# Kernel optimization log

Measured on AMD Instinct MI355X. Metric: run time of the kernel, lower is better.

The kernel has to match this reference:

```python
import jax, jax.numpy as jnp
import numpy as np

N, E, F_IN, F_EDGE, HID, OUT = 100000, 1600000, 128, 8, 128, 2
BN_EPS = 1e-5


def setup_inputs() -> dict:
    key = jax.random.key(0)
    ks = jax.random.split(key, 16)
    rn = lambda k, shape, s=0.05: jax.random.normal(k, shape, jnp.float32) * s
    return {
        "x": jax.random.normal(ks[0], (N, F_IN), jnp.float32),
        "edge_attr": jax.random.uniform(ks[1], (E, F_EDGE), dtype=jnp.float32),
        "edge_index": jax.random.randint(ks[2], (2, E), 0, N, jnp.int32),
        # edge MLP: Linear(F_EDGE, HID) -> ReLU -> Linear(HID, 1) -> Sigmoid
        "ew1_w": rn(ks[3], (F_EDGE, HID)), "ew1_b": jnp.zeros((HID,), jnp.float32),
        "ew2_w": rn(ks[4], (HID, 1)), "ew2_b": jnp.zeros((1,), jnp.float32),
        # SAGEConv layers: lin_l (on aggregated neighbors, with bias) + lin_r (root)
        "w1_l": rn(ks[5], (F_IN, HID)), "b1_l": jnp.zeros((HID,), jnp.float32), "w1_r": rn(ks[6], (F_IN, HID)),
        "w2_l": rn(ks[7], (HID, HID)), "b2_l": jnp.zeros((HID,), jnp.float32), "w2_r": rn(ks[8], (HID, HID)),
        "w3_l": rn(ks[9], (HID, OUT)), "b3_l": jnp.zeros((OUT,), jnp.float32), "w3_r": rn(ks[10], (HID, OUT)),
        # BatchNorm1d (eval mode: running stats)
        "bn1_g": jnp.ones((HID,), jnp.float32), "bn1_b": jnp.zeros((HID,), jnp.float32),
        "bn1_m": rn(ks[11], (HID,), 0.01), "bn1_v": jnp.ones((HID,), jnp.float32),
        "bn2_g": jnp.ones((HID,), jnp.float32), "bn2_b": jnp.zeros((HID,), jnp.float32),
        "bn2_m": rn(ks[12], (HID,), 0.01), "bn2_v": jnp.ones((HID,), jnp.float32),
    }


def _sage(x, src, dst, ew, w_l, b_l, w_r):
    # PyG SAGEConv(aggr='mean'): msg = x[src] * edge_weight, mean over incoming edges at dst
    msg = x[src] * ew[:, None]                                  # [E, F]
    s = jax.ops.segment_sum(msg, dst, num_segments=N)           # [N, F]
    deg = jax.ops.segment_sum(jnp.ones((src.shape[0],), x.dtype), dst, num_segments=N)
    agg = s / jnp.maximum(deg, 1.0)[:, None]
    return agg @ w_l + b_l + x @ w_r


def _bn_eval(h, g, b, m, v):
    return (h - m) * jax.lax.rsqrt(v + BN_EPS) * g + b


def reference(x, edge_attr, edge_index,
              ew1_w, ew1_b, ew2_w, ew2_b,
              w1_l, b1_l, w1_r, w2_l, b2_l, w2_r, w3_l, b3_l, w3_r,
              bn1_g, bn1_b, bn1_m, bn1_v, bn2_g, bn2_b, bn2_m, bn2_v):
    src, dst = edge_index[0], edge_index[1]
    # per-edge scalar weight from small MLP
    ew = jax.nn.sigmoid(jax.nn.relu(edge_attr @ ew1_w + ew1_b) @ ew2_w + ew2_b).reshape(-1)
    h = _sage(x, src, dst, ew, w1_l, b1_l, w1_r)
    h = jax.nn.relu(_bn_eval(h, bn1_g, bn1_b, bn1_m, bn1_v))    # dropout no-op in eval
    h = _sage(h, src, dst, ew, w2_l, b2_l, w2_r)
    h = jax.nn.relu(_bn_eval(h, bn2_g, bn2_b, bn2_m, bn2_v))
    return _sage(h, src, dst, ew, w3_l, b3_l, w3_r)
```

## Files before the change

### kernel.cpp

```cpp
#include <hip/hip_runtime.h>
#include <math.h>

#define N_NODES 100000
#define N_EDGES 1600000
#define F_INF   128
#define HIDF    128

typedef __attribute__((ext_vector_type(8)))  short short8;
typedef __attribute__((ext_vector_type(16))) float floatx16;

__device__ __forceinline__ unsigned short f2bf(float f) {
    unsigned u = __float_as_uint(f);
    return (unsigned short)((u + 0x7FFFu + ((u >> 16) & 1u)) >> 16);
}

__global__ __launch_bounds__(256) void k_edge_mlp(
        const float* __restrict__ ea,
        const float* __restrict__ w1, const float* __restrict__ b1,
        const float* __restrict__ w2, const float* __restrict__ b2,
        float* __restrict__ ew) {
    const int lane = threadIdx.x & 63;
    const int cl   = lane & 31;
    const int half = lane >> 5;
    const int wid  = blockIdx.x * (blockDim.x >> 6) + (threadIdx.x >> 6);
    const int nw   = gridDim.x * (blockDim.x >> 6);

    short8 bw[4];
    float  w2c[4];
#pragma unroll
    for (int cb = 0; cb < 4; ++cb) {
        const int n = cb * 32 + cl;
        short8 b;
        if (half == 0) {
#pragma unroll
            for (int j = 0; j < 8; ++j) b[j] = (short)f2bf(w1[j * 128 + n]);
        } else {
            b[0] = (short)f2bf(b1[n]);
#pragma unroll
            for (int j = 1; j < 8; ++j) b[j] = 0;
        }
        bw[cb] = b;
        w2c[cb] = w2[n];
    }
    short8 Abias;
    Abias[0] = (short)0x3F80;
#pragma unroll
    for (int j = 1; j < 8; ++j) Abias[j] = 0;

    floatx16 czero;
#pragma unroll
    for (int r = 0; r < 16; ++r) czero[r] = 0.f;

    const float bias2 = b2[0];

    for (int e0 = wid * 32; e0 < N_EDGES; e0 += nw * 32) {
        short8 Ah;
        if (half == 0) {
            const float4 a0 = *(const float4*)(ea + (size_t)(e0 + cl) * 8);
            const float4 a1 = *(const float4*)(ea + (size_t)(e0 + cl) * 8 + 4);
            Ah[0] = (short)f2bf(a0.x); Ah[1] = (short)f2bf(a0.y);
            Ah[2] = (short)f2bf(a0.z); Ah[3] = (short)f2bf(a0.w);
            Ah[4] = (short)f2bf(a1.x); Ah[5] = (short)f2bf(a1.y);
            Ah[6] = (short)f2bf(a1.z); Ah[7] = (short)f2bf(a1.w);
        } else {
            Ah = Abias;
        }

        float z[16];
#pragma unroll
        for (int r = 0; r < 16; ++r) z[r] = 0.f;

#pragma unroll
        for (int cb = 0; cb < 4; ++cb) {
            floatx16 acc = __builtin_amdgcn_mfma_f32_32x32x16_bf16(Ah, bw[cb], czero, 0, 0, 0);
#pragma unroll
            for (int r = 0; r < 16; ++r)
                z[r] = fmaf(fmaxf(acc[r], 0.f), w2c[cb], z[r]);
        }

#pragma unroll
        for (int m = 1; m <= 16; m <<= 1) {
#pragma unroll
            for (int r = 0; r < 16; ++r) z[r] += __shfl_xor(z[r], m, 64);
        }

        float zz = z[0];
#pragma unroll
        for (int r = 1; r < 16; ++r) zz = (cl == r) ? z[r] : zz;
        if (cl < 16) {
            const int row = (cl & 3) + 8 * (cl >> 2) + 4 * half;
            ew[e0 + row] = 1.f / (1.f + __expf(-(zz + bias2)));
        }
    }
}

__global__ void k_deg(const int* __restrict__ dst, int* __restrict__ deg,
                      unsigned char* __restrict__ rank) {
    int e = blockIdx.x * 256 + threadIdx.x;
    if (e < N_EDGES) rank[e] = (unsigned char)atomicAdd(&deg[dst[e]], 1);
}

__global__ void k_scan1(const int* __restrict__ deg, int* __restrict__ incl,
                        int* __restrict__ bsum) {
    __shared__ int sm[1024];
    const int tid = threadIdx.x;
    const int gi  = blockIdx.x * 1024 + tid;
    int v = (gi < N_NODES) ? deg[gi] : 0;
    sm[tid] = v;
    __syncthreads();
    for (int off = 1; off < 1024; off <<= 1) {
        int t = (tid >= off) ? sm[tid - off] : 0;
        __syncthreads();
        sm[tid] += t;
        __syncthreads();
    }
    if (gi < N_NODES) incl[gi] = sm[tid];
    if (tid == 1023) bsum[blockIdx.x] = sm[1023];
}

__global__ void k_scan2(const int* __restrict__ bsum, int* __restrict__ boff, int nb) {
    __shared__ int sm[128];
    const int tid = threadIdx.x;
    int v = (tid < nb) ? bsum[tid] : 0;
    sm[tid] = v;
    __syncthreads();
    for (int off = 1; off < 128; off <<= 1) {
        int t = (tid >= off) ? sm[tid - off] : 0;
        __syncthreads();
        sm[tid] += t;
        __syncthreads();
    }
    boff[tid] = sm[tid] - v;
}

__global__ void k_scan3(const int* __restrict__ incl, const int* __restrict__ boff,
                        int* __restrict__ rowptr) {
    int i = blockIdx.x * 256 + threadIdx.x;
    if (i < N_NODES) rowptr[i + 1] = boff[i >> 10] + incl[i];
    if (i == 0) rowptr[0] = 0;
}

__global__ void k_fill(const int* __restrict__ src, const int* __restrict__ dst,
                       const float* __restrict__ ew, const int* __restrict__ rowptr,
                       const unsigned char* __restrict__ rank,
                       unsigned* __restrict__ cw) {
    int e = blockIdx.x * 256 + threadIdx.x;
    if (e < N_EDGES) {
        int d   = dst[e];
        int pos = rowptr[d] + (int)rank[e];
        unsigned wb = (unsigned)f2bf(ew[e]) & 0x7FFFu;
        cw[pos] = ((unsigned)src[e] << 15) | wb;
    }
}

__global__ void k_cast(const float* __restrict__ x, unsigned short* __restrict__ xb) {
    const int i = (blockIdx.x * 256 + threadIdx.x) * 4;
    const float4 v = *(const float4*)(x + i);
    ushort4 o;
    o.x = f2bf(v.x); o.y = f2bf(v.y); o.z = f2bf(v.z); o.w = f2bf(v.w);
    *(ushort4*)(xb + i) = o;
}

__global__ __launch_bounds__(256) void k_agg16(
        const unsigned short* __restrict__ xb, const int* __restrict__ rowptr,
        const unsigned* __restrict__ cw, float* __restrict__ aggout) {
    const int lane = threadIdx.x & 63;
    const int half = lane >> 5;
    const int cl   = lane & 31;
    const int node = blockIdx.x * (blockDim.x >> 6) + (threadIdx.x >> 6);
    if (node >= N_NODES) return;
    const int s = rowptr[node], e = rowptr[node + 1];
    float a0 = 0.f, a1 = 0.f, a2 = 0.f, a3 = 0.f;

    for (int j0 = s; j0 < e; j0 += 8) {
        int ss[4]; float ww[4];
#pragma unroll
        for (int u = 0; u < 4; ++u) {
            const int j  = j0 + 2 * u + half;
            const int jc = min(j, e - 1);
            const unsigned p = cw[jc];
            ss[u] = (int)(p >> 15);
            ww[u] = (j < e) ? __uint_as_float((p & 0x7FFFu) << 16) : 0.f;
        }
        uint2 g[4];
#pragma unroll
        for (int u = 0; u < 4; ++u)
            g[u] = *(const uint2*)(xb + (size_t)ss[u] * 128 + cl * 4);
#pragma unroll
        for (int u = 0; u < 4; ++u) {
            const float f0 = __uint_as_float(g[u].x << 16);
            const float f1 = __uint_as_float(g[u].x & 0xFFFF0000u);
            const float f2 = __uint_as_float(g[u].y << 16);
            const float f3 = __uint_as_float(g[u].y & 0xFFFF0000u);
            a0 = fmaf(ww[u], f0, a0);
            a1 = fmaf(ww[u], f1, a1);
            a2 = fmaf(ww[u], f2, a2);
            a3 = fmaf(ww[u], f3, a3);
        }
    }
    a0 += __shfl_xor(a0, 32, 64);
    a1 += __shfl_xor(a1, 32, 64);
    a2 += __shfl_xor(a2, 32, 64);
    a3 += __shfl_xor(a3, 32, 64);
    if (half == 0) {
        const float inv = 1.f / fmaxf((float)(e - s), 1.f);
        float4 r;
        r.x = a0 * inv; r.y = a1 * inv; r.z = a2 * inv; r.w = a3 * inv;
        *(float4*)(aggout + (size_t)node * 128 + cl * 4) = r;
    }
}

__global__ void k_wpack(const float* __restrict__ Wl, const float* __restrict__ Wr,
                        short* __restrict__ Whi, short* __restrict__ Wlo) {
    int idx = blockIdx.x * 256 + threadIdx.x;
    int j  = idx & 7;
    int L  = (idx >> 3) & 63;
    int cb = (idx >> 9) & 3;
    int kb = (idx >> 11);
    int k  = kb * 16 + (L >> 5) * 8 + j;
    int n  = cb * 32 + (L & 31);
    float a = (k < 128) ? Wl[k * 128 + n] : Wr[(k - 128) * 128 + n];
    unsigned short hb = f2bf(a);
    float hf = __uint_as_float((unsigned)hb << 16);
    Whi[idx] = (short)hb;
    Wlo[idx] = (short)f2bf(a - hf);
}

__global__ __launch_bounds__(256) void k_gemm_mfma(
    const float* __restrict__ Aagg, const float* __restrict__ Ax,
    const short* __restrict__ Whi, const short* __restrict__ Wlo,
    const float* __restrict__ bl,
    const float* __restrict__ bng, const float* __restrict__ bnb,
    const float* __restrict__ bnm, const float* __restrict__ bnv,
    float* __restrict__ out, unsigned short* __restrict__ out16) {
    const int tid  = threadIdx.x;
    const int lane = tid & 63;
    const int w    = tid >> 6;
    const int row0 = blockIdx.x * 128 + w * 32;
    const int rrow = lane & 31;
    const int kq   = lane >> 5;
    const int arow = min(row0 + rrow, N_NODES - 1);

    floatx16 acc[4];
#pragma unroll
    for (int cb = 0; cb < 4; ++cb)
#pragma unroll
        for (int r = 0; r < 16; ++r) acc[cb][r] = 0.f;

    const float* Abase0 = Aagg + (size_t)arow * 128 + kq * 8;
    const float* Abase1 = Ax   + (size_t)arow * 128 + kq * 8;

#pragma unroll 2
    for (int kb = 0; kb < 16; ++kb) {
        const float* ap = ((kb < 8) ? Abase0 : Abase1) + (kb & 7) * 16;
        const float4 a0 = *(const float4*)(ap);
        const float4 a1 = *(const float4*)(ap + 4);
        const float av[8] = {a0.x, a0.y, a0.z, a0.w, a1.x, a1.y, a1.z, a1.w};
        short8 Ah, Al;
#pragma unroll
        for (int j = 0; j < 8; ++j) {
            unsigned short hb = f2bf(av[j]);
            float hf = __uint_as_float((unsigned)hb << 16);
            Ah[j] = (short)hb;
            Al[j] = (short)f2bf(av[j] - hf);
        }
#pragma unroll
        for (int cb = 0; cb < 4; ++cb) {
            const size_t wo = ((size_t)(kb * 4 + cb) * 64 + lane) * 8;
            const short8 wh = *(const short8*)(Whi + wo);
            const short8 wl = *(const short8*)(Wlo + wo);
            acc[cb] = __builtin_amdgcn_mfma_f32_32x32x16_bf16(Ah, wh, acc[cb], 0, 0, 0);
            acc[cb] = __builtin_amdgcn_mfma_f32_32x32x16_bf16(Al, wh, acc[cb], 0, 0, 0);
            acc[cb] = __builtin_amdgcn_mfma_f32_32x32x16_bf16(Ah, wl, acc[cb], 0, 0, 0);
        }
    }

#pragma unroll
    for (int cb = 0; cb < 4; ++cb) {
        const int c = cb * 32 + (lane & 31);
        const float s = bng[c] * rsqrtf(bnv[c] + 1e-5f);
        const float t = (bl[c] - bnm[c]) * s + bnb[c];
#pragma unroll
        for (int r = 0; r < 16; ++r) {
            const int row = row0 + (r & 3) + 8 * (r >> 2) + 4 * kq;
            if (row < N_NODES) {
                const float v = fmaxf(fmaf(acc[cb][r], s, t), 0.f);
                out[(size_t)row * 128 + c] = v;
                if (out16) out16[(size_t)row * 128 + c] = f2bf(v);
            }
        }
    }
}

__global__ void k_lin3(const float* __restrict__ h, const float* __restrict__ w3l,
                       const float* __restrict__ w3r, float* __restrict__ t4) {
    const int lane = threadIdx.x & 63;
    const int node = blockIdx.x * (blockDim.x >> 6) + (threadIdx.x >> 6);
    if (node >= N_NODES) return;
    float h0 = h[(size_t)node * 128 + lane];
    float h1 = h[(size_t)node * 128 + 64 + lane];
    float2 wl0 = *(const float2*)(w3l + lane * 2);
    float2 wl1 = *(const float2*)(w3l + (64 + lane) * 2);
    float2 wr0 = *(const float2*)(w3r + lane * 2);
    float2 wr1 = *(const float2*)(w3r + (64 + lane) * 2);
    float p0 = h0 * wl0.x + h1 * wl1.x;
    float p1 = h0 * wl0.y + h1 * wl1.y;
    float p2 = h0 * wr0.x + h1 * wr1.x;
    float p3 = h0 * wr0.y + h1 * wr1.y;
#pragma unroll
    for (int m = 1; m < 64; m <<= 1) {
        p0 += __shfl_xor(p0, m, 64);
        p1 += __shfl_xor(p1, m, 64);
        p2 += __shfl_xor(p2, m, 64);
        p3 += __shfl_xor(p3, m, 64);
    }
    if (lane == 0) {
        float4 o; o.x = p0; o.y = p1; o.z = p2; o.w = p3;
        *(float4*)(t4 + (size_t)node * 4) = o;
    }
}

__global__ void k_out(const float* __restrict__ t4, const int* __restrict__ rowptr,
                      const unsigned* __restrict__ cw,
                      const float* __restrict__ b3, float* __restrict__ out) {
    const int lane = threadIdx.x & 63;
    const int node = blockIdx.x * (blockDim.x >> 6) + (threadIdx.x >> 6);
    if (node >= N_NODES) return;
    const int s = rowptr[node], e = rowptr[node + 1];
    float a0 = 0.f, a1 = 0.f;
    for (int j = s + lane; j < e; j += 64) {
        const unsigned p = cw[j];
        const int   sr = (int)(p >> 15);
        const float w  = __uint_as_float((p & 0x7FFFu) << 16);
        float2 t = *(const float2*)(t4 + (size_t)sr * 4);
        a0 += w * t.x; a1 += w * t.y;
    }
#pragma unroll
    for (int m = 1; m < 64; m <<= 1) {
        a0 += __shfl_xor(a0, m, 64);
        a1 += __shfl_xor(a1, m, 64);
    }
    if (lane == 0) {
        float inv = 1.f / fmaxf((float)(e - s), 1.f);
        float2 o;
        o.x = a0 * inv + b3[0] + t4[(size_t)node * 4 + 2];
        o.y = a1 * inv + b3[1] + t4[(size_t)node * 4 + 3];
        *(float2*)(out + (size_t)node * 2) = o;
    }
}

extern "C" void kernel_launch(void* const* d_in, const int* in_sizes, int n_in,
                              void* d_out, int out_size, void* d_ws, size_t ws_size,
                              hipStream_t stream) {
    const float* x    = (const float*)d_in[0];
    const float* ea   = (const float*)d_in[1];
    const int*   ei   = (const int*)d_in[2];
    const float* ew1w = (const float*)d_in[3];
    const float* ew1b = (const float*)d_in[4];
    const float* ew2w = (const float*)d_in[5];
    const float* ew2b = (const float*)d_in[6];
    const float* w1l  = (const float*)d_in[7];
    const float* b1l  = (const float*)d_in[8];
    const float* w1r  = (const float*)d_in[9];
    const float* w2l  = (const float*)d_in[10];
    const float* b2l  = (const float*)d_in[11];
    const float* w2r  = (const float*)d_in[12];
    const float* w3l  = (const float*)d_in[13];
    const float* b3l  = (const float*)d_in[14];
    const float* w3r  = (const float*)d_in[15];
    const float* bn1g = (const float*)d_in[16];
    const float* bn1b = (const float*)d_in[17];
    const float* bn1m = (const float*)d_in[18];
    const float* bn1v = (const float*)d_in[19];
    const float* bn2g = (const float*)d_in[20];
    const float* bn2b = (const float*)d_in[21];
    const float* bn2m = (const float*)d_in[22];
    const float* bn2v = (const float*)d_in[23];

    const int* src = ei;
    const int* dst = ei + N_EDGES;
    float* out = (float*)d_out;

    size_t off = 0;
    auto carve = [&](size_t bytes) -> void* {
        void* p = (char*)d_ws + off;
        off += (bytes + 255) & ~(size_t)255;
        return p;
    };
    float* ew     = (float*)carve((size_t)N_EDGES * 4);
    unsigned* cw  = (unsigned*)carve((size_t)N_EDGES * 4);
    unsigned char* rank = (unsigned char*)carve((size_t)N_EDGES);
    int*   rowptr = (int*)carve((size_t)(N_NODES + 1) * 4);
    int*   deg    = (int*)carve((size_t)N_NODES * 4);
    int*   bsum   = (int*)carve(128 * 4);
    int*   boff   = (int*)carve(128 * 4);
    int*   incl   = (int*)carve((size_t)N_NODES * 4);
    float* agg    = (float*)carve((size_t)N_NODES * 128 * 4);
    float* hA     = (float*)carve((size_t)N_NODES * 128 * 4);
    float* hB     = (float*)carve((size_t)N_NODES * 128 * 4);
    float* t4     = (float*)carve((size_t)N_NODES * 4 * 4);
    short* W1hi   = (short*)carve(32768 * 2);
    short* W1lo   = (short*)carve(32768 * 2);
    short* W2hi   = (short*)carve(32768 * 2);
    short* W2lo   = (short*)carve(32768 * 2);
    unsigned short* xb   = (unsigned short*)carve((size_t)N_NODES * 128 * 2);
    unsigned short* hA16 = (unsigned short*)carve((size_t)N_NODES * 128 * 2);
    (void)ws_size; (void)n_in; (void)in_sizes; (void)out_size;

    hipMemsetAsync(deg, 0, (size_t)N_NODES * 4, stream);

    const int EB = (N_EDGES + 255) / 256;
    const int NB_SCAN = (N_NODES + 1023) / 1024;
    const int NWB = (N_NODES + 3) / 4;
    const int GB = (N_NODES + 127) / 128;
    const int CB = (N_NODES * 128 / 4 + 255) / 256;

    k_deg<<<EB, 256, 0, stream>>>(dst, deg, rank);
    k_cast<<<CB, 256, 0, stream>>>(x, xb);
    k_edge_mlp<<<2048, 256, 0, stream>>>(ea, ew1w, ew1b, ew2w, ew2b, ew);
    k_wpack<<<128, 256, 0, stream>>>(w1l, w1r, W1hi, W1lo);
    k_wpack<<<128, 256, 0, stream>>>(w2l, w2r, W2hi, W2lo);
    k_scan1<<<NB_SCAN, 1024, 0, stream>>>(deg, incl, bsum);
    k_scan2<<<1, 128, 0, stream>>>(bsum, boff, NB_SCAN);
    k_scan3<<<(N_NODES + 255) / 256, 256, 0, stream>>>(incl, boff, rowptr);
    k_fill<<<EB, 256, 0, stream>>>(src, dst, ew, rowptr, rank, cw);

    k_agg16<<<NWB, 256, 0, stream>>>(xb, rowptr, cw, agg);
    k_gemm_mfma<<<GB, 256, 0, stream>>>(agg, x, W1hi, W1lo, b1l,
                                        bn1g, bn1b, bn1m, bn1v, hA, hA16);
    k_agg16<<<NWB, 256, 0, stream>>>(hA16, rowptr, cw, agg);
    k_gemm_mfma<<<GB, 256, 0, stream>>>(agg, hA, W2hi, W2lo, b2l,
                                        bn2g, bn2b, bn2m, bn2v, hB, nullptr);
    k_lin3<<<NWB, 256, 0, stream>>>(hB, w3l, w3r, t4);
    k_out<<<NWB, 256, 0, stream>>>(t4, rowptr, cw, b3l, out);
}
```

Before: 591.5 us.

## Fuse front-end kernels and store activations as split bf16 hi/lo pairs

Merges the degree count, x cast, edge MLP and both weight packs into one heterogeneous kernel that dispatches on block index. Scan2 and scan3 are merged into one kernel. All intermediate activations (agg, hA, hB) are now stored as bf16 hi/lo pairs instead of fp32, so the GEMM loads ready-made MFMA operands and no longer converts them. The goals are fewer launches and less conversion work inside the GEMM. Total bytes are roughly unchanged, and the fused kernel mixes workloads that may balance unevenly.

New measurement: 562.6 us. 4.9% less time.

```diff
diff --git a/kernel.cpp b/kernel.cpp
--- a/kernel.cpp
+++ b/kernel.cpp
@@ -6,6 +6,11 @@
 #define F_INF   128
 #define HIDF    128
 
+#define MLP_BLOCKS  2048
+#define CAST_BLOCKS 12500
+#define WP_BASE     (CAST_BLOCKS + MLP_BLOCKS)
+#define FRONT_GRID  (WP_BASE + 256)
+
 typedef __attribute__((ext_vector_type(8)))  short short8;
 typedef __attribute__((ext_vector_type(16))) float floatx16;
 
@@ -13,17 +18,70 @@
     unsigned u = __float_as_uint(f);
     return (unsigned short)((u + 0x7FFFu + ((u >> 16) & 1u)) >> 16);
 }
-
-__global__ __launch_bounds__(256) void k_edge_mlp(
+__device__ __forceinline__ float bf2f(unsigned short h) {
+    return __uint_as_float((unsigned)h << 16);
+}
+
+__global__ __launch_bounds__(256) void k_front(
+        const float* __restrict__ x,
+        unsigned short* __restrict__ xbHi, unsigned short* __restrict__ xbLo,
+        const int* __restrict__ dst, int* __restrict__ deg,
+        unsigned char* __restrict__ rank,
         const float* __restrict__ ea,
-        const float* __restrict__ w1, const float* __restrict__ b1,
-        const float* __restrict__ w2, const float* __restrict__ b2,
-        float* __restrict__ ew) {
+        const float* __restrict__ mw1, const float* __restrict__ mb1,
+        const float* __restrict__ mw2, const float* __restrict__ mb2,
+        float* __restrict__ ew,
+        const float* __restrict__ w1l, const float* __restrict__ w1r,
+        short* __restrict__ W1hi, short* __restrict__ W1lo,
+        const float* __restrict__ w2l, const float* __restrict__ w2r,
+        short* __restrict__ W2hi, short* __restrict__ W2lo) {
+    const int bid = blockIdx.x;
+
+    if (bid >= WP_BASE) {
+        const int wb  = bid - WP_BASE;
+        const int idx = (wb & 127) * 256 + threadIdx.x;
+        const float* Wl = (wb < 128) ? w1l : w2l;
+        const float* Wr = (wb < 128) ? w1r : w2r;
+        short* Whi = (wb < 128) ? W1hi : W2hi;
+        short* Wlo = (wb < 128) ? W1lo : W2lo;
+        const int j  = idx & 7;
+        const int L  = (idx >> 3) & 63;
+        const int cb = (idx >> 9) & 3;
+        const int kb = (idx >> 11);
+        const int k  = kb * 16 + (L >> 5) * 8 + j;
+        const int n  = cb * 32 + (L & 31);
+        const float a = (k < 128) ? Wl[k * 128 + n] : Wr[(k - 128) * 128 + n];
+        const unsigned short hb = f2bf(a);
+        Whi[idx] = (short)hb;
+        Wlo[idx] = (short)f2bf(a - bf2f(hb));
+        return;
+    }
+
+    const bool is_mlp = ((bid % 7) == 3) && (bid < 7 * MLP_BLOCKS);
+    if (!is_mlp) {
+        const int c   = (bid < 4) ? 0 : min(MLP_BLOCKS, (bid - 4) / 7 + 1);
+        const int gid = (bid - c) * 256 + (int)threadIdx.x;
+        const int i   = gid * 4;
+        const float4 v = *(const float4*)(x + i);
+        ushort4 h, l;
+        h.x = f2bf(v.x); l.x = f2bf(v.x - bf2f(h.x));
+        h.y = f2bf(v.y); l.y = f2bf(v.y - bf2f(h.y));
+        h.z = f2bf(v.z); l.z = f2bf(v.z - bf2f(h.z));
+        h.w = f2bf(v.w); l.w = f2bf(v.w - bf2f(h.w));
+        *(ushort4*)(xbHi + i) = h;
+        *(ushort4*)(xbLo + i) = l;
+        if ((gid & 1) == 0) {
+            const int e = gid >> 1;
+            rank[e] = (unsigned char)atomicAdd(&deg[dst[e]], 1);
+        }
+        return;
+    }
+
     const int lane = threadIdx.x & 63;
     const int cl   = lane & 31;
     const int half = lane >> 5;
-    const int wid  = blockIdx.x * (blockDim.x >> 6) + (threadIdx.x >> 6);
-    const int nw   = gridDim.x * (blockDim.x >> 6);
+    const int wid  = (bid / 7) * 4 + ((int)threadIdx.x >> 6);
+    const int nw   = MLP_BLOCKS * 4;
 
     short8 bw[4];
     float  w2c[4];
@@ -33,14 +91,14 @@
         short8 b;
         if (half == 0) {
 #pragma unroll
-            for (int j = 0; j < 8; ++j) b[j] = (short)f2bf(w1[j * 128 + n]);
+            for (int j = 0; j < 8; ++j) b[j] = (short)f2bf(mw1[j * 128 + n]);
         } else {
-            b[0] = (short)f2bf(b1[n]);
+            b[0] = (short)f2bf(mb1[n]);
 #pragma unroll
             for (int j = 1; j < 8; ++j) b[j] = 0;
         }
         bw[cb] = b;
-        w2c[cb] = w2[n];
+        w2c[cb] = mw2[n];
     }
     short8 Abias;
     Abias[0] = (short)0x3F80;
@@ -51,7 +109,7 @@
 #pragma unroll
     for (int r = 0; r < 16; ++r) czero[r] = 0.f;
 
-    const float bias2 = b2[0];
+    const float bias2 = mb2[0];
 
     for (int e0 = wid * 32; e0 < N_EDGES; e0 += nw * 32) {
         short8 Ah;
@@ -92,12 +150,6 @@
             ew[e0 + row] = 1.f / (1.f + __expf(-(zz + bias2)));
         }
     }
-}
-
-__global__ void k_deg(const int* __restrict__ dst, int* __restrict__ deg,
-                      unsigned char* __restrict__ rank) {
-    int e = blockIdx.x * 256 + threadIdx.x;
-    if (e < N_EDGES) rank[e] = (unsigned char)atomicAdd(&deg[dst[e]], 1);
 }
 
 __global__ void k_scan1(const int* __restrict__ deg, int* __restrict__ incl,
@@ -118,25 +170,27 @@
     if (tid == 1023) bsum[blockIdx.x] = sm[1023];
 }
 
-__global__ void k_scan2(const int* __restrict__ bsum, int* __restrict__ boff, int nb) {
+__global__ void k_scan23(const int* __restrict__ incl, const int* __restrict__ bsum,
+                         int* __restrict__ rowptr, int nb) {
     __shared__ int sm[128];
     const int tid = threadIdx.x;
-    int v = (tid < nb) ? bsum[tid] : 0;
-    sm[tid] = v;
+    int v = 0;
+    if (tid < 128) {
+        v = (tid < nb) ? bsum[tid] : 0;
+        sm[tid] = v;
+    }
     __syncthreads();
     for (int off = 1; off < 128; off <<= 1) {
-        int t = (tid >= off) ? sm[tid - off] : 0;
+        int t = 0;
+        if (tid < 128 && tid >= off) t = sm[tid - off];
         __syncthreads();
-        sm[tid] += t;
+        if (tid < 128) sm[tid] += t;
         __syncthreads();
     }
-    boff[tid] = sm[tid] - v;
-}
-
-__global__ void k_scan3(const int* __restrict__ incl, const int* __restrict__ boff,
-                        int* __restrict__ rowptr) {
-    int i = blockIdx.x * 256 + threadIdx.x;
-    if (i < N_NODES) rowptr[i + 1] = boff[i >> 10] + incl[i];
+    if (tid < 128) sm[tid] -= v;
+    __syncthreads();
+    const int i = blockIdx.x * 256 + tid;
+    if (i < N_NODES) rowptr[i + 1] = sm[i >> 10] + incl[i];
     if (i == 0) rowptr[0] = 0;
 }
 
@@ -153,17 +207,10 @@
     }
 }
 
-__global__ void k_cast(const float* __restrict__ x, unsigned short* __restrict__ xb) {
-    const int i = (blockIdx.x * 256 + threadIdx.x) * 4;
-    const float4 v = *(const float4*)(x + i);
-    ushort4 o;
-    o.x = f2bf(v.x); o.y = f2bf(v.y); o.z = f2bf(v.z); o.w = f2bf(v.w);
-    *(ushort4*)(xb + i) = o;
-}
-
 __global__ __launch_bounds__(256) void k_agg16(
         const unsigned short* __restrict__ xb, const int* __restrict__ rowptr,
-        const unsigned* __restrict__ cw, float* __restrict__ aggout) {
+        const unsigned* __restrict__ cw,
+        unsigned short* __restrict__ aggHi, unsigned short* __restrict__ aggLo) {
     const int lane = threadIdx.x & 63;
     const int half = lane >> 5;
     const int cl   = lane & 31;
@@ -204,35 +251,25 @@
     a3 += __shfl_xor(a3, 32, 64);
     if (half == 0) {
         const float inv = 1.f / fmaxf((float)(e - s), 1.f);
-        float4 r;
-        r.x = a0 * inv; r.y = a1 * inv; r.z = a2 * inv; r.w = a3 * inv;
-        *(float4*)(aggout + (size_t)node * 128 + cl * 4) = r;
-    }
-}
-
-__global__ void k_wpack(const float* __restrict__ Wl, const float* __restrict__ Wr,
-                        short* __restrict__ Whi, short* __restrict__ Wlo) {
-    int idx = blockIdx.x * 256 + threadIdx.x;
-    int j  = idx & 7;
-    int L  = (idx >> 3) & 63;
-    int cb = (idx >> 9) & 3;
-    int kb = (idx >> 11);
-    int k  = kb * 16 + (L >> 5) * 8 + j;
-    int n  = cb * 32 + (L & 31);
-    float a = (k < 128) ? Wl[k * 128 + n] : Wr[(k - 128) * 128 + n];
-    unsigned short hb = f2bf(a);
-    float hf = __uint_as_float((unsigned)hb << 16);
-    Whi[idx] = (short)hb;
-    Wlo[idx] = (short)f2bf(a - hf);
-}
-
-__global__ __launch_bounds__(256) void k_gemm_mfma(
-    const float* __restrict__ Aagg, const float* __restrict__ Ax,
+        a0 *= inv; a1 *= inv; a2 *= inv; a3 *= inv;
+        ushort4 h, l;
+        h.x = f2bf(a0); l.x = f2bf(a0 - bf2f(h.x));
+        h.y = f2bf(a1); l.y = f2bf(a1 - bf2f(h.y));
+        h.z = f2bf(a2); l.z = f2bf(a2 - bf2f(h.z));
+        h.w = f2bf(a3); l.w = f2bf(a3 - bf2f(h.w));
+        *(ushort4*)(aggHi + (size_t)node * 128 + cl * 4) = h;
+        *(ushort4*)(aggLo + (size_t)node * 128 + cl * 4) = l;
+    }
+}
+
+__global__ __launch_bounds__(256) void k_gemm(
+    const unsigned short* __restrict__ AaggHi, const unsigned short* __restrict__ AaggLo,
+    const unsigned short* __restrict__ AxHi, const unsigned short* __restrict__ AxLo,
     const short* __restrict__ Whi, const short* __restrict__ Wlo,
     const float* __restrict__ bl,
     const float* __restrict__ bng, const float* __restrict__ bnb,
     const float* __restrict__ bnm, const float* __restrict__ bnv,
-    float* __restrict__ out, unsigned short* __restrict__ out16) {
+    unsigned short* __restrict__ outHi, unsigned short* __restrict__ outLo) {
     const int tid  = threadIdx.x;
     const int lane = tid & 63;
     const int w    = tid >> 6;
@@ -247,23 +284,13 @@
 #pragma unroll
         for (int r = 0; r < 16; ++r) acc[cb][r] = 0.f;
 
-    const float* Abase0 = Aagg + (size_t)arow * 128 + kq * 8;
-    const float* Abase1 = Ax   + (size_t)arow * 128 + kq * 8;
+    const size_t abase = (size_t)arow * 128 + kq * 8;
 
 #pragma unroll 2
     for (int kb = 0; kb < 16; ++kb) {
-        const float* ap = ((kb < 8) ? Abase0 : Abase1) + (kb & 7) * 16;
-        const float4 a0 = *(const float4*)(ap);
-        const float4 a1 = *(const float4*)(ap + 4);
-        const float av[8] = {a0.x, a0.y, a0.z, a0.w, a1.x, a1.y, a1.z, a1.w};
-        short8 Ah, Al;
-#pragma unroll
-        for (int j = 0; j < 8; ++j) {
-            unsigned short hb = f2bf(av[j]);
-            float hf = __uint_as_float((unsigned)hb << 16);
-            Ah[j] = (short)hb;
-            Al[j] = (short)f2bf(av[j] - hf);
-        }
+        const size_t ao = abase + (kb & 7) * 16;
+        const short8 Ah = *(const short8*)(((kb < 8) ? AaggHi : AxHi) + ao);
+        const short8 Al = *(const short8*)(((kb < 8) ? AaggLo : AxLo) + ao);
 #pragma unroll
         for (int cb = 0; cb < 4; ++cb) {
             const size_t wo = ((size_t)(kb * 4 + cb) * 64 + lane) * 8;
@@ -285,24 +312,28 @@
             const int row = row0 + (r & 3) + 8 * (r >> 2) + 4 * kq;
             if (row < N_NODES) {
                 const float v = fmaxf(fmaf(acc[cb][r], s, t), 0.f);
-                out[(size_t)row * 128 + c] = v;
-                if (out16) out16[(size_t)row * 128 + c] = f2bf(v);
+                const unsigned short hb = f2bf(v);
+                outHi[(size_t)row * 128 + c] = hb;
+                outLo[(size_t)row * 128 + c] = f2bf(v - bf2f(hb));
             }
         }
     }
 }
 
-__global__ void k_lin3(const float* __restrict__ h, const float* __restrict__ w3l,
+__global__ void k_lin3(const unsigned short* __restrict__ hHi,
+                       const unsigned short* __restrict__ hLo,
+                       const float* __restrict__ w3l,
                        const float* __restrict__ w3r, float* __restrict__ t4) {
     const int lane = threadIdx.x & 63;
     const int node = blockIdx.x * (blockDim.x >> 6) + (threadIdx.x >> 6);
     if (node >= N_NODES) return;
-    float h0 = h[(size_t)node * 128 + lane];
-    float h1 = h[(size_t)node * 128 + 64 + lane];
-    float2 wl0 = *(const float2*)(w3l + lane * 2);
-    float2 wl1 = *(const float2*)(w3l + (64 + lane) * 2);
-    float2 wr0 = *(const float2*)(w3r + lane * 2);
-    float2 wr1 = *(const float2*)(w3r + (64 + lane) * 2);
+    const size_t b = (size_t)node * 128;
+    const float h0 = bf2f(hHi[b + lane])      + bf2f(hLo[b + lane]);
+    const float h1 = bf2f(hHi[b + 64 + lane]) + bf2f(hLo[b + 64 + lane]);
+    const float2 wl0 = *(const float2*)(w3l + lane * 2);
+    const float2 wl1 = *(const float2*)(w3l + (64 + lane) * 2);
+    const float2 wr0 = *(const float2*)(w3r + lane * 2);
+    const float2 wr1 = *(const float2*)(w3r + (64 + lane) * 2);
     float p0 = h0 * wl0.x + h1 * wl1.x;
     float p1 = h0 * wl0.y + h1 * wl1.y;
     float p2 = h0 * wr0.x + h1 * wr1.x;
@@ -393,18 +424,20 @@
     int*   rowptr = (int*)carve((size_t)(N_NODES + 1) * 4);
     int*   deg    = (int*)carve((size_t)N_NODES * 4);
     int*   bsum   = (int*)carve(128 * 4);
-    int*   boff   = (int*)carve(128 * 4);
     int*   incl   = (int*)carve((size_t)N_NODES * 4);
-    float* agg    = (float*)carve((size_t)N_NODES * 128 * 4);
-    float* hA     = (float*)carve((size_t)N_NODES * 128 * 4);
-    float* hB     = (float*)carve((size_t)N_NODES * 128 * 4);
     float* t4     = (float*)carve((size_t)N_NODES * 4 * 4);
     short* W1hi   = (short*)carve(32768 * 2);
     short* W1lo   = (short*)carve(32768 * 2);
     short* W2hi   = (short*)carve(32768 * 2);
     short* W2lo   = (short*)carve(32768 * 2);
-    unsigned short* xb   = (unsigned short*)carve((size_t)N_NODES * 128 * 2);
-    unsigned short* hA16 = (unsigned short*)carve((size_t)N_NODES * 128 * 2);
+    unsigned short* xbHi  = (unsigned short*)carve((size_t)N_NODES * 128 * 2);
+    unsigned short* xbLo  = (unsigned short*)carve((size_t)N_NODES * 128 * 2);
+    unsigned short* aggHi = (unsigned short*)carve((size_t)N_NODES * 128 * 2);
+    unsigned short* aggLo = (unsigned short*)carve((size_t)N_NODES * 128 * 2);
+    unsigned short* hHi   = (unsigned short*)carve((size_t)N_NODES * 128 * 2);
+    unsigned short* hLo   = (unsigned short*)carve((size_t)N_NODES * 128 * 2);
+    unsigned short* hBhi  = (unsigned short*)carve((size_t)N_NODES * 128 * 2);
+    unsigned short* hBlo  = (unsigned short*)carve((size_t)N_NODES * 128 * 2);
     (void)ws_size; (void)n_in; (void)in_sizes; (void)out_size;
 
     hipMemsetAsync(deg, 0, (size_t)N_NODES * 4, stream);
@@ -413,24 +446,21 @@
     const int NB_SCAN = (N_NODES + 1023) / 1024;
     const int NWB = (N_NODES + 3) / 4;
     const int GB = (N_NODES + 127) / 128;
-    const int CB = (N_NODES * 128 / 4 + 255) / 256;
-
-    k_deg<<<EB, 256, 0, stream>>>(dst, deg, rank);
-    k_cast<<<CB, 256, 0, stream>>>(x, xb);
-    k_edge_mlp<<<2048, 256, 0, stream>>>(ea, ew1w, ew1b, ew2w, ew2b, ew);
-    k_wpack<<<128, 256, 0, stream>>>(w1l, w1r, W1hi, W1lo);
-    k_wpack<<<128, 256, 0, stream>>>(w2l, w2r, W2hi, W2lo);
+
+    k_front<<<FRONT_GRID, 256, 0, stream>>>(
+        x, xbHi, xbLo, dst, deg, rank,
+        ea, ew1w, ew1b, ew2w, ew2b, ew,
+        w1l, w1r, W1hi, W1lo, w2l, w2r, W2hi, W2lo);
     k_scan1<<<NB_SCAN, 1024, 0, stream>>>(deg, incl, bsum);
-    k_scan2<<<1, 128, 0, stream>>>(bsum, boff, NB_SCAN);
-    k_scan3<<<(N_NODES + 255) / 256, 256, 0, stream>>>(incl, boff, rowptr);
+    k_scan23<<<(N_NODES + 255) / 256, 256, 0, stream>>>(incl, bsum, rowptr, NB_SCAN);
     k_fill<<<EB, 256, 0, stream>>>(src, dst, ew, rowptr, rank, cw);
 
-    k_agg16<<<NWB, 256, 0, stream>>>(xb, rowptr, cw, agg);
-    k_gemm_mfma<<<GB, 256, 0, stream>>>(agg, x, W1hi, W1lo, b1l,
-                                        bn1g, bn1b, bn1m, bn1v, hA, hA16);
-    k_agg16<<<NWB, 256, 0, stream>>>(hA16, rowptr, cw, agg);
-    k_gemm_mfma<<<GB, 256, 0, stream>>>(agg, hA, W2hi, W2lo, b2l,
-                                        bn2g, bn2b, bn2m, bn2v, hB, nullptr);
-    k_lin3<<<NWB, 256, 0, stream>>>(hB, w3l, w3r, t4);
+    k_agg16<<<NWB, 256, 0, stream>>>(xbHi, rowptr, cw, aggHi, aggLo);
+    k_gemm<<<GB, 256, 0, stream>>>(aggHi, aggLo, xbHi, xbLo, W1hi, W1lo, b1l,
+                                   bn1g, bn1b, bn1m, bn1v, hHi, hLo);
+    k_agg16<<<NWB, 256, 0, stream>>>(hHi, rowptr, cw, aggHi, aggLo);
+    k_gemm<<<GB, 256, 0, stream>>>(aggHi, aggLo, hHi, hLo, W2hi, W2lo, b2l,
+                                   bn2g, bn2b, bn2m, bn2v, hBhi, hBlo);
+    k_lin3<<<NWB, 256, 0, stream>>>(hBhi, hBlo, w3l, w3r, t4);
     k_out<<<NWB, 256, 0, stream>>>(t4, rowptr, cw, b3l, out);
 }
```
